# Optimization experiments

Hardware: AMD Instinct MI355X
Metric: run time of the kernel (lower is better)

Reference implementation:

```python
import jax, jax.numpy as jnp
import numpy as np

NEG_SLOPE = 0.01  # nn.LeakyReLU default

def _leaky(x):
    return jnp.where(x >= 0, x, NEG_SLOPE * x)

def setup_inputs() -> dict:
    key = jax.random.key(0)
    ks = jax.random.split(key, 8)
    in_ch = 64
    B, H, W = 8, 256, 256
    x = jax.random.normal(ks[0], (B, 2 * in_ch, H, W), dtype=jnp.float32)
    dims = [(64, 128), (32, 64), (16, 32), (8, 16), (4, 8), (2, 4), (1, 2)]
    inp = {"x": x}
    for i, (o, c) in enumerate(dims):
        # kaiming_normal_ fan_out, relu: std = sqrt(2 / fan_out), fan_out = o*1*1
        std = np.sqrt(2.0 / o).astype(np.float32)
        inp[f"w{i+1}"] = jax.random.normal(ks[i + 1], (o, c), dtype=jnp.float32) * std
    return inp

def reference(x, w1, w2, w3, w4, w5, w6, w7):
    # Each 1x1 conv (bias-free) is a per-pixel matmul over channels.
    h = x
    for w in (w1, w2, w3, w4, w5, w6):
        h = _leaky(jnp.einsum('bchw,oc->bohw', h, w))
    out = jnp.einsum('bchw,oc->bohw', h, w7)  # final conv, no activation
    return out
```

## Files before the change

### kernel.cpp

```cpp
#include <hip/hip_runtime.h>


#define NEG_SLOPE 0.01f

__global__ void pack_w_kernel(const float* __restrict__ w1, const float* __restrict__ w2,
                              const float* __restrict__ w3, const float* __restrict__ w4,
                              const float* __restrict__ w5, const float* __restrict__ w6,
                              const float* __restrict__ w7, float* __restrict__ wt) {
    const float* ws[7] = {w1, w2, w3, w4, w5, w6, w7};
    const int O[7] = {64, 32, 16, 8, 4, 2, 1};
    const int C[7] = {128, 64, 32, 16, 8, 4, 2};
    int t  = blockIdx.x * blockDim.x + threadIdx.x;
    int nt = gridDim.x * blockDim.x;
    int off = 0;
    for (int l = 0; l < 7; ++l) {
        int n = O[l] * C[l];
        for (int i = t; i < n; i += nt) {
            int c = i / O[l];
            int o = i - c * O[l];
            wt[off + i] = ws[l][o * C[l] + c];
        }
        off += n;
    }
}

__device__ __forceinline__ float leaky(float v) { return v >= 0.f ? v : NEG_SLOPE * v; }

template <int CIN, int COUT>
__device__ __forceinline__ void dense(const float* __restrict__ wt,
                                      const float* __restrict__ in,
                                      float* __restrict__ out, bool act) {
#pragma unroll
    for (int o = 0; o < COUT; ++o) out[o] = 0.f;
#pragma unroll
    for (int c = 0; c < CIN; ++c) {
        float xv = in[c];
#pragma unroll
        for (int o = 0; o < COUT; ++o) out[o] = fmaf(wt[c * COUT + o], xv, out[o]);
    }
    if (act) {
#pragma unroll
        for (int o = 0; o < COUT; ++o) out[o] = leaky(out[o]);
    }
}

__global__ __launch_bounds__(256) void fused_chain_kernel(const float* __restrict__ x,
                                                          const float* __restrict__ wt,
                                                          float* __restrict__ out) {
    constexpr int HW = 65536;
    int g = blockIdx.x * 256 + threadIdx.x;
    int b = g >> 16;
    int p = g & (HW - 1);
    const float* xb = x + (size_t)b * 128 * HW + p;

    float h1[64];
#pragma unroll
    for (int o = 0; o < 64; ++o) h1[o] = 0.f;
    for (int c = 0; c < 128; ++c) {
        float xv = xb[(size_t)c * HW];
        const float* wc = wt + c * 64;
#pragma unroll
        for (int o = 0; o < 64; ++o) h1[o] = fmaf(wc[o], xv, h1[o]);
    }
#pragma unroll
    for (int o = 0; o < 64; ++o) h1[o] = leaky(h1[o]);

    float h2[32];
    dense<64, 32>(wt + 8192, h1, h2, true);
    float h3[16];
    dense<32, 16>(wt + 10240, h2, h3, true);
    float h4[8];
    dense<16, 8>(wt + 10752, h3, h4, true);
    float h5[4];
    dense<8, 4>(wt + 10880, h4, h5, true);
    float h6[2];
    dense<4, 2>(wt + 10912, h5, h6, true);

    out[g] = fmaf(wt[10920], h6[0], wt[10921] * h6[1]);
}

extern "C" void kernel_launch(void* const* d_in, const int* in_sizes, int n_in,
                              void* d_out, int out_size, void* d_ws, size_t ws_size,
                              hipStream_t stream) {
    const float* x  = (const float*)d_in[0];
    const float* w1 = (const float*)d_in[1];
    const float* w2 = (const float*)d_in[2];
    const float* w3 = (const float*)d_in[3];
    const float* w4 = (const float*)d_in[4];
    const float* w5 = (const float*)d_in[5];
    const float* w6 = (const float*)d_in[6];
    const float* w7 = (const float*)d_in[7];
    float* out = (float*)d_out;
    float* wt  = (float*)d_ws;

    pack_w_kernel<<<32, 256, 0, stream>>>(w1, w2, w3, w4, w5, w6, w7, wt);

    const int P = 8 * 256 * 256;
    fused_chain_kernel<<<P / 256, 256, 0, stream>>>(x, wt, out);
}
```

Measured before the change: 425.7 us.

## Run first three 1x1 conv layers on bf16 MFMA with LDS-staged activations

Replaces the per-thread scalar FMA chain with bf16 16x16x32 MFMA instructions for the first three layers. Each wave processes 64 pixels, stages intermediate activations through LDS in bf16, and finishes the small tail layers in fp32 from LDS-cached weights. The separate weight-packing kernel is removed because weights are loaded directly into MFMA A-fragments. This targets the FMA-bound compute of the original kernel, at the cost of bf16 rounding of inputs and activations, which may affect accuracy.

```diff
diff --git a/kernel.cpp b/kernel.cpp
--- a/kernel.cpp
+++ b/kernel.cpp
@@ -3,80 +3,180 @@
 
 #define NEG_SLOPE 0.01f
 
-__global__ void pack_w_kernel(const float* __restrict__ w1, const float* __restrict__ w2,
-                              const float* __restrict__ w3, const float* __restrict__ w4,
-                              const float* __restrict__ w5, const float* __restrict__ w6,
-                              const float* __restrict__ w7, float* __restrict__ wt) {
-    const float* ws[7] = {w1, w2, w3, w4, w5, w6, w7};
-    const int O[7] = {64, 32, 16, 8, 4, 2, 1};
-    const int C[7] = {128, 64, 32, 16, 8, 4, 2};
-    int t  = blockIdx.x * blockDim.x + threadIdx.x;
-    int nt = gridDim.x * blockDim.x;
-    int off = 0;
-    for (int l = 0; l < 7; ++l) {
-        int n = O[l] * C[l];
-        for (int i = t; i < n; i += nt) {
-            int c = i / O[l];
-            int o = i - c * O[l];
-            wt[off + i] = ws[l][o * C[l] + c];
-        }
-        off += n;
-    }
-}
+typedef __attribute__((ext_vector_type(8))) short bf16x8;
+typedef __attribute__((ext_vector_type(4))) float f32x4;
 
 __device__ __forceinline__ float leaky(float v) { return v >= 0.f ? v : NEG_SLOPE * v; }
 
-template <int CIN, int COUT>
-__device__ __forceinline__ void dense(const float* __restrict__ wt,
-                                      const float* __restrict__ in,
-                                      float* __restrict__ out, bool act) {
-#pragma unroll
-    for (int o = 0; o < COUT; ++o) out[o] = 0.f;
-#pragma unroll
-    for (int c = 0; c < CIN; ++c) {
-        float xv = in[c];
-#pragma unroll
-        for (int o = 0; o < COUT; ++o) out[o] = fmaf(wt[c * COUT + o], xv, out[o]);
-    }
-    if (act) {
-#pragma unroll
-        for (int o = 0; o < COUT; ++o) out[o] = leaky(out[o]);
-    }
+__device__ __forceinline__ short f2b(float f) {
+    unsigned u = __float_as_uint(f);
+    u += 0x7fffu + ((u >> 16) & 1u);
+    return (short)(u >> 16);
 }
 
-__global__ __launch_bounds__(256) void fused_chain_kernel(const float* __restrict__ x,
-                                                          const float* __restrict__ wt,
-                                                          float* __restrict__ out) {
+__device__ __forceinline__ unsigned pk(float a, float b) {
+    return (unsigned)(unsigned short)f2b(a) | ((unsigned)(unsigned short)f2b(b) << 16);
+}
+
+__device__ __forceinline__ bf16x8 loadA(const float* __restrict__ wsrc, int C, int m, int k) {
+    const float* pr = wsrc + m * C + k;
+    f32x4 lo = *(const f32x4*)pr;
+    f32x4 hi = *(const f32x4*)(pr + 4);
+    bf16x8 r;
+    r[0] = f2b(lo[0]); r[1] = f2b(lo[1]); r[2] = f2b(lo[2]); r[3] = f2b(lo[3]);
+    r[4] = f2b(hi[0]); r[5] = f2b(hi[1]); r[6] = f2b(hi[2]); r[7] = f2b(hi[3]);
+    return r;
+}
+
+__global__ __launch_bounds__(256) void fused_mfma_kernel(
+    const float* __restrict__ x,
+    const float* __restrict__ w1, const float* __restrict__ w2,
+    const float* __restrict__ w3, const float* __restrict__ w4,
+    const float* __restrict__ w5, const float* __restrict__ w6,
+    const float* __restrict__ w7, float* __restrict__ out) {
     constexpr int HW = 65536;
-    int g = blockIdx.x * 256 + threadIdx.x;
-    int b = g >> 16;
-    int p = g & (HW - 1);
-    const float* xb = x + (size_t)b * 128 * HW + p;
 
-    float h1[64];
+    __shared__ short lds_h1[4][16 * 72];
+    __shared__ short lds_h2[4][16 * 40];
+    __shared__ float lds_h3[4][64 * 17];
+    __shared__ float lds_tw[176];
+
+    const int tid = threadIdx.x;
+    if (tid < 128)      lds_tw[tid] = w4[tid];
+    else if (tid < 160) lds_tw[tid] = w5[tid - 128];
+    else if (tid < 168) lds_tw[tid] = w6[tid - 160];
+    else if (tid < 170) lds_tw[tid] = w7[tid - 168];
+    __syncthreads();
+
+    const int w    = tid >> 6;
+    const int lane = tid & 63;
+    const int p    = lane & 15;
+    const int q    = lane >> 4;
+
+    const int px0   = blockIdx.x * 256 + w * 64;
+    const int batch = px0 >> 16;
+    const int pin   = px0 & (HW - 1);
+    const float* xb = x + (size_t)batch * 128 * HW;
+
+    bf16x8 a1[4][4];
 #pragma unroll
-    for (int o = 0; o < 64; ++o) h1[o] = 0.f;
-    for (int c = 0; c < 128; ++c) {
-        float xv = xb[(size_t)c * HW];
-        const float* wc = wt + c * 64;
+    for (int Mt = 0; Mt < 4; ++Mt)
 #pragma unroll
-        for (int o = 0; o < 64; ++o) h1[o] = fmaf(wc[o], xv, h1[o]);
+        for (int Ks = 0; Ks < 4; ++Ks)
+            a1[Mt][Ks] = loadA(w1, 128, Mt * 16 + p, Ks * 32 + q * 8);
+    bf16x8 a2[2][2];
+#pragma unroll
+    for (int Mt = 0; Mt < 2; ++Mt)
+#pragma unroll
+        for (int Ks = 0; Ks < 2; ++Ks)
+            a2[Mt][Ks] = loadA(w2, 64, Mt * 16 + p, Ks * 32 + q * 8);
+    bf16x8 a3 = loadA(w3, 32, p, q * 8);
+
+#pragma unroll
+    for (int Nt = 0; Nt < 4; ++Nt) {
+        const float* xp = xb + pin + Nt * 16 + p;
+
+        bf16x8 bx[4];
+#pragma unroll
+        for (int Ks = 0; Ks < 4; ++Ks) {
+            float t[8];
+#pragma unroll
+            for (int j = 0; j < 8; ++j)
+                t[j] = xp[(size_t)(Ks * 32 + q * 8 + j) * HW];
+#pragma unroll
+            for (int j = 0; j < 8; ++j) bx[Ks][j] = f2b(t[j]);
+        }
+
+        f32x4 d1[4];
+#pragma unroll
+        for (int Mt = 0; Mt < 4; ++Mt) {
+            f32x4 acc = {0.f, 0.f, 0.f, 0.f};
+#pragma unroll
+            for (int Ks = 0; Ks < 4; ++Ks)
+                acc = __builtin_amdgcn_mfma_f32_16x16x32_bf16(a1[Mt][Ks], bx[Ks], acc, 0, 0, 0);
+            d1[Mt] = acc;
+        }
+
+        {
+            short* h1w = &lds_h1[w][p * 72];
+#pragma unroll
+            for (int Mt = 0; Mt < 4; ++Mt) {
+                uint2 v;
+                v.x = pk(leaky(d1[Mt][0]), leaky(d1[Mt][1]));
+                v.y = pk(leaky(d1[Mt][2]), leaky(d1[Mt][3]));
+                *(uint2*)(h1w + Mt * 16 + q * 4) = v;
+            }
+        }
+
+        bf16x8 b2[2];
+#pragma unroll
+        for (int Ks = 0; Ks < 2; ++Ks)
+            b2[Ks] = *(const bf16x8*)&lds_h1[w][p * 72 + Ks * 32 + q * 8];
+
+        f32x4 d2[2];
+#pragma unroll
+        for (int Mt = 0; Mt < 2; ++Mt) {
+            f32x4 acc = {0.f, 0.f, 0.f, 0.f};
+#pragma unroll
+            for (int Ks = 0; Ks < 2; ++Ks)
+                acc = __builtin_amdgcn_mfma_f32_16x16x32_bf16(a2[Mt][Ks], b2[Ks], acc, 0, 0, 0);
+            d2[Mt] = acc;
+        }
+
+        {
+            short* h2w = &lds_h2[w][p * 40];
+#pragma unroll
+            for (int Mt = 0; Mt < 2; ++Mt) {
+                uint2 v;
+                v.x = pk(leaky(d2[Mt][0]), leaky(d2[Mt][1]));
+                v.y = pk(leaky(d2[Mt][2]), leaky(d2[Mt][3]));
+                *(uint2*)(h2w + Mt * 16 + q * 4) = v;
+            }
+        }
+
+        bf16x8 b3 = *(const bf16x8*)&lds_h2[w][p * 40 + q * 8];
+        f32x4 zero = {0.f, 0.f, 0.f, 0.f};
+        f32x4 d3 = __builtin_amdgcn_mfma_f32_16x16x32_bf16(a3, b3, zero, 0, 0, 0);
+
+        {
+            float* h3w = &lds_h3[w][(Nt * 16 + p) * 17 + q * 4];
+            h3w[0] = leaky(d3[0]);
+            h3w[1] = leaky(d3[1]);
+            h3w[2] = leaky(d3[2]);
+            h3w[3] = leaky(d3[3]);
+        }
     }
+
+    const float* h3r = &lds_h3[w][lane * 17];
+    float h[16];
 #pragma unroll
-    for (int o = 0; o < 64; ++o) h1[o] = leaky(h1[o]);
+    for (int c = 0; c < 16; ++c) h[c] = h3r[c];
 
-    float h2[32];
-    dense<64, 32>(wt + 8192, h1, h2, true);
-    float h3[16];
-    dense<32, 16>(wt + 10240, h2, h3, true);
-    float h4[8];
-    dense<16, 8>(wt + 10752, h3, h4, true);
-    float h5[4];
-    dense<8, 4>(wt + 10880, h4, h5, true);
-    float h6[2];
-    dense<4, 2>(wt + 10912, h5, h6, true);
-
-    out[g] = fmaf(wt[10920], h6[0], wt[10921] * h6[1]);
+    float g4[8];
+#pragma unroll
+    for (int o = 0; o < 8; ++o) {
+        float a = 0.f;
+#pragma unroll
+        for (int c = 0; c < 16; ++c) a = fmaf(lds_tw[o * 16 + c], h[c], a);
+        g4[o] = leaky(a);
+    }
+    float g5[4];
+#pragma unroll
+    for (int o = 0; o < 4; ++o) {
+        float a = 0.f;
+#pragma unroll
+        for (int c = 0; c < 8; ++c) a = fmaf(lds_tw[128 + o * 8 + c], g4[c], a);
+        g5[o] = leaky(a);
+    }
+    float g6[2];
+#pragma unroll
+    for (int o = 0; o < 2; ++o) {
+        float a = 0.f;
+#pragma unroll
+        for (int c = 0; c < 4; ++c) a = fmaf(lds_tw[160 + o * 4 + c], g5[c], a);
+        g6[o] = leaky(a);
+    }
+    out[px0 + lane] = fmaf(lds_tw[168], g6[0], lds_tw[169] * g6[1]);
 }
 
 extern "C" void kernel_launch(void* const* d_in, const int* in_sizes, int n_in,
@@ -91,10 +191,7 @@
     const float* w6 = (const float*)d_in[6];
     const float* w7 = (const float*)d_in[7];
     float* out = (float*)d_out;
-    float* wt  = (float*)d_ws;
-
-    pack_w_kernel<<<32, 256, 0, stream>>>(w1, w2, w3, w4, w5, w6, w7, wt);
 
     const int P = 8 * 256 * 256;
-    fused_chain_kernel<<<P / 256, 256, 0, stream>>>(x, wt, out);
+    fused_mfma_kernel<<<P / 256, 256, 0, stream>>>(x, w1, w2, w3, w4, w5, w6, w7, out);
 }
```

Measured after the change: 439.7 us. 1.03x slower.
